# Kernel tuning notes

Hardware: AMD Instinct MI355X
Metric: run time of the kernel (lower is better)

Reference implementation:

```python
import jax, jax.numpy as jnp
import numpy as np
from jax import lax

B, S, D, H = 4, 1024, 1024, 16
DK = D // H


def setup_inputs() -> dict:
    key = jax.random.key(0)
    ks = jax.random.split(key, 8)
    s = 0.02
    return {
        "text_embeddings": jax.random.normal(ks[0], (B, S, D), jnp.float32),
        "text_mask": jnp.ones((B, S), jnp.int32),
        "W_G": jax.random.normal(ks[1], (D, D), jnp.float32) * s,
        "b_G": jnp.zeros((D,), jnp.float32),
        "Wq": jax.random.normal(ks[2], (D, D), jnp.float32) * s,
        "bq": jnp.zeros((D,), jnp.float32),
        "Wk": jax.random.normal(ks[3], (D, D), jnp.float32) * s,
        "bk": jnp.zeros((D,), jnp.float32),
        "conv_w": jax.random.normal(ks[4], (D, H, 3), jnp.float32) * s,
        "conv_b": jnp.zeros((D,), jnp.float32),
    }


def _rope_tables(seq_len, dk):
    # interleaved sinusoidal tables, each value repeated twice along feature dim
    pos = jnp.arange(seq_len, dtype=jnp.float32)[:, None]            # [S,1]
    inv = jnp.power(10000.0, -2.0 * jnp.arange(dk // 2, dtype=jnp.float32) / dk)
    ang = pos * inv                                                   # [S,DK/2]
    cos_pos = jnp.repeat(jnp.cos(ang), 2, axis=-1)[None, None]        # [1,1,S,DK]
    sin_pos = jnp.repeat(jnp.sin(ang), 2, axis=-1)[None, None]
    return cos_pos, sin_pos


def reference(text_embeddings, text_mask, W_G, b_G, Wq, bq, Wk, bk, conv_w, conv_b):
    b, s, d = text_embeddings.shape
    g = text_embeddings @ W_G + b_G                                   # [B,S,D]
    q = (g @ Wq + bq).reshape(b, s, H, DK).transpose(0, 2, 1, 3)      # [B,H,S,DK]
    k = (g @ Wk + bk).reshape(b, s, H, DK).transpose(0, 2, 1, 3)

    cos_pos, sin_pos = _rope_tables(s, DK)
    # NOTE: query rotation uses +q_odd (module does NOT negate for q), key uses -k_odd
    qw2 = jnp.stack([q[..., 1::2], q[..., ::2]], axis=-1).reshape(q.shape)
    qw = q * cos_pos + qw2 * sin_pos
    kw2 = jnp.stack([-k[..., 1::2], k[..., ::2]], axis=-1).reshape(k.shape)
    kw = k * cos_pos + kw2 * sin_pos

    scores = jnp.einsum("bhqd,bhkd->bhqk", qw, kw) / np.float32(np.sqrt(DK))
    mask = text_mask[:, None, None, :]                                # [B,1,1,S]
    scores = jnp.where(mask == 0, jnp.float32(-1e9), scores)
    p_attn = jax.nn.softmax(scores, axis=-1)                          # [B,H,S,S]

    row0 = p_attn[:, :, 0, :]                                         # [B,H,S]
    conv = lax.conv_general_dilated(
        row0, conv_w, window_strides=(1,), padding=[(1, 1)],
        dimension_numbers=("NCH", "OIH", "NCH"))                      # [B,D,S]
    return jax.nn.relu(conv + conv_b[None, :, None])
```

## Files before the change

### kernel.cpp

```cpp
#include <hip/hip_runtime.h>
#include <math.h>

#define B_  4
#define S_  1024
#define D_  1024
#define H_  16
#define DK_ 64
#define M_  (B_ * S_)

typedef __bf16 bf16x8 __attribute__((ext_vector_type(8)));
typedef float  f32x4  __attribute__((ext_vector_type(4)));

__device__ __forceinline__ unsigned short f2bf(float f) {
  unsigned u = __builtin_bit_cast(unsigned, f);
  u = (u + 0x7FFFu + ((u >> 16) & 1u)) >> 16;
  return (unsigned short)u;
}
__device__ __forceinline__ float bf2f(unsigned short h) {
  unsigned u = ((unsigned)h) << 16;
  return __builtin_bit_cast(float, u);
}

__device__ __forceinline__ void gl_lds16(const void* g, void* lds) {
  __builtin_amdgcn_global_load_lds(
      (const __attribute__((address_space(1))) unsigned int*)(unsigned long long)g,
      (__attribute__((address_space(3))) unsigned int*)(unsigned int)(unsigned long long)lds,
      16, 0, 0);
}

__global__ __launch_bounds__(256) void prep_kernel(
    const float* __restrict__ X, const float* __restrict__ W_G,
    const float* __restrict__ Wk, const float* __restrict__ bG,
    unsigned short* __restrict__ WGbf, unsigned short* __restrict__ WkT,
    float* __restrict__ partG, float* __restrict__ partB) {
  __shared__ float tle[32][33];
  __shared__ float gs2[4][32];
  __shared__ float bgs[32];
  const int blk = blockIdx.x;
  const int tid = threadIdx.x;

  if (blk < 512) {
    const int i = (blk * 256 + tid) * 2;
    const float4 v0 = ((const float4*)W_G)[i];
    const float4 v1 = ((const float4*)W_G)[i + 1];
    ushort4 h0, h1;
    h0.x = f2bf(v0.x); h0.y = f2bf(v0.y); h0.z = f2bf(v0.z); h0.w = f2bf(v0.w);
    h1.x = f2bf(v1.x); h1.y = f2bf(v1.y); h1.z = f2bf(v1.z); h1.w = f2bf(v1.w);
    ((ushort4*)WGbf)[i] = h0;
    ((ushort4*)WGbf)[i + 1] = h1;
  } else if (blk < 1536) {
    const int t = blk - 512;
    const int k0 = (t & 31) * 32;
    const int n0 = (t >> 5) * 32;
    const int tx = tid & 31;
    const int ty = tid >> 5;
#pragma unroll
    for (int r = 0; r < 32; r += 8)
      tle[ty + r][tx] = Wk[(size_t)(k0 + ty + r) * 1024 + n0 + tx];
    __syncthreads();
#pragma unroll
    for (int r = 0; r < 32; r += 8)
      WkT[(size_t)(n0 + ty + r) * 1024 + k0 + tx] = f2bf(tle[tx][ty + r]);
  } else if (blk < 1664) {
    const int bl = blk - 1536;
    const int sg = bl >> 2;
    const int mg = bl & 3;
    if (tid < 128) {
      const int b = tid >> 5, kk = tid & 31;
      gs2[b][kk] = X[(size_t)b * S_ * D_ + sg * 32 + kk];
    }
    __syncthreads();
    const int mid = mg * 256 + tid;
    float a0 = 0.f, a1 = 0.f, a2 = 0.f, a3 = 0.f;
#pragma unroll
    for (int kk = 0; kk < 32; ++kk) {
      const float w = W_G[(size_t)(sg * 32 + kk) * 1024 + mid];
      a0 = fmaf(gs2[0][kk], w, a0);
      a1 = fmaf(gs2[1][kk], w, a1);
      a2 = fmaf(gs2[2][kk], w, a2);
      a3 = fmaf(gs2[3][kk], w, a3);
    }
    partG[(size_t)(sg * 4 + 0) * 1024 + mid] = a0;
    partG[(size_t)(sg * 4 + 1) * 1024 + mid] = a1;
    partG[(size_t)(sg * 4 + 2) * 1024 + mid] = a2;
    partG[(size_t)(sg * 4 + 3) * 1024 + mid] = a3;
  } else {
    const int bl = blk - 1664;
    const int sl = bl >> 2;
    const int ng = bl & 3;
    if (tid < 32) bgs[tid] = bG[sl * 32 + tid];
    __syncthreads();
    const int n = ng * 256 + tid;
    float a = 0.f;
#pragma unroll
    for (int kk = 0; kk < 32; ++kk)
      a = fmaf(bgs[kk], Wk[(size_t)(sl * 32 + kk) * 1024 + n], a);
    partB[(size_t)sl * 1024 + n] = a;
  }
}

#define GM 64
#define GN 128

__global__ __launch_bounds__(256) void gemm_bf16(
    const unsigned short* __restrict__ A, const unsigned short* __restrict__ BT,
    const float* __restrict__ bias, unsigned short* __restrict__ C,
    const int mShift, const int nGemmBlocks,
    const float* __restrict__ Wq, float* __restrict__ part,
    const float* __restrict__ partG, const float* __restrict__ bG,
    const float* __restrict__ partB, const float* __restrict__ bk,
    float* __restrict__ biasK,
    const float* __restrict__ X, unsigned short* __restrict__ Xbf,
    float* __restrict__ tab,
    const float* __restrict__ bq, const int* __restrict__ mask,
    float* __restrict__ scores, float* __restrict__ mS) {
  __shared__ __align__(16) unsigned short As[2][GM * 32];
  __shared__ __align__(16) unsigned short Bs[2][GN * 32];
  __shared__ float gs[4][32];
  __shared__ float q0s[128];
  __shared__ float sc[64][9];

  const int flat = blockIdx.x;
  const int tid  = threadIdx.x;

  if (flat >= nGemmBlocks) {
    const int eb = flat - nGemmBlocks;
    if (eb < 128) {
      const int slab = eb >> 2;
      const int n = (eb & 3) * 256 + tid;
      if (tid < 128) {
        const int b = tid >> 5, kk = tid & 31;
        float v = bG[slab * 32 + kk];
        const float* pg = partG + (size_t)b * 1024 + slab * 32 + kk;
#pragma unroll
        for (int sg = 0; sg < 32; ++sg) v += pg[(size_t)sg * 4096];
        gs[b][kk] = v;
      }
      __syncthreads();
      float a0 = 0.f, a1 = 0.f, a2 = 0.f, a3 = 0.f;
#pragma unroll
      for (int kk = 0; kk < 32; ++kk) {
        const float w = Wq[(size_t)(slab * 32 + kk) * D_ + n];
        a0 = fmaf(gs[0][kk], w, a0);
        a1 = fmaf(gs[1][kk], w, a1);
        a2 = fmaf(gs[2][kk], w, a2);
        a3 = fmaf(gs[3][kk], w, a3);
      }
      part[(size_t)(slab * 4 + 0) * D_ + n] = a0;
      part[(size_t)(slab * 4 + 1) * D_ + n] = a1;
      part[(size_t)(slab * 4 + 2) * D_ + n] = a2;
      part[(size_t)(slab * 4 + 3) * D_ + n] = a3;
    } else if (eb < 132) {
      const int n = (eb - 128) * 256 + tid;
      float v = bk[n];
#pragma unroll
      for (int sl = 0; sl < 32; ++sl) v += partB[(size_t)sl * 1024 + n];
      biasK[n] = v;
    } else if (eb < 260) {
      const int idx = (eb - 132) * 256 + tid;
      const int s = idx >> 5, j = idx & 31;
      const float inv = (float)exp(-(double)j * (9.210340371976182736 / 32.0));
      float sn, c;
      sincosf((float)s * inv, &sn, &c);
      tab[(size_t)s * 64 + 2 * j] = c;
      tab[(size_t)s * 64 + 2 * j + 1] = sn;
    } else {
      const int i = ((eb - 260) * 256 + tid) * 2;
      const float4 v0 = ((const float4*)X)[i];
      const float4 v1 = ((const float4*)X)[i + 1];
      ushort4 h0, h1;
      h0.x = f2bf(v0.x); h0.y = f2bf(v0.y); h0.z = f2bf(v0.z); h0.w = f2bf(v0.w);
      h1.x = f2bf(v1.x); h1.y = f2bf(v1.y); h1.z = f2bf(v1.z); h1.w = f2bf(v1.w);
      ((ushort4*)Xbf)[i] = h0;
      ((ushort4*)Xbf)[i + 1] = h1;
    }
    return;
  }

  const int bx = flat >> mShift;
  const int by = flat & ((1 << mShift) - 1);
  const int wv   = tid >> 6;
  const int lane = tid & 63;
  const int m0 = by * GM;
  const int n0 = bx * GN;

  if (scores && tid < 128) {
    const int nq = n0 + tid;
    float v = bq[nq];
#pragma unroll
    for (int sl2 = 0; sl2 < 32; ++sl2)
      v += part[(size_t)(sl2 * 4 + (m0 >> 10)) * D_ + nq];
    q0s[tid] = v;
  }

  const int colOff = (lane & 3) * 8;
  const size_t aOff  = (size_t)(m0 + 16 * wv + (lane >> 2)) * 1024 + colOff;
  const size_t bOff0 = (size_t)(n0 + 32 * wv + (lane >> 2)) * 1024 + colOff;
  const size_t bOff1 = bOff0 + (size_t)16 * 1024;

  const int l15  = lane & 15;
  const int quad = lane >> 4;

  f32x4 acc[4][2];
#pragma unroll
  for (int i = 0; i < 4; ++i)
#pragma unroll
    for (int j = 0; j < 2; ++j) acc[i][j] = (f32x4){0.f, 0.f, 0.f, 0.f};

#pragma unroll 1
  for (int k0 = 0; k0 < 1024; k0 += 64) {
    __syncthreads();
#pragma unroll
    for (int ks = 0; ks < 2; ++ks) {
      gl_lds16(A  + aOff  + k0 + ks * 32, &As[ks][wv * 512]);
      gl_lds16(BT + bOff0 + k0 + ks * 32, &Bs[ks][wv * 1024]);
      gl_lds16(BT + bOff1 + k0 + ks * 32, &Bs[ks][wv * 1024 + 512]);
    }
    __syncthreads();

#pragma unroll
    for (int ks = 0; ks < 2; ++ks) {
      bf16x8 af[4], bfr[2];
#pragma unroll
      for (int mi = 0; mi < 4; ++mi)
        af[mi] = *(const bf16x8*)(&As[ks][(mi * 16 + l15) * 32 + quad * 8]);
#pragma unroll
      for (int ni = 0; ni < 2; ++ni)
        bfr[ni] =
            *(const bf16x8*)(&Bs[ks][(wv * 32 + ni * 16 + l15) * 32 + quad * 8]);
#pragma unroll
      for (int mi = 0; mi < 4; ++mi)
#pragma unroll
        for (int ni = 0; ni < 2; ++ni)
          acc[mi][ni] = __builtin_amdgcn_mfma_f32_16x16x32_bf16(
              af[mi], bfr[ni], acc[mi][ni], 0, 0, 0);
    }
  }

  if (scores) {
    const int b_i   = m0 >> 10;
    const int sbase = m0 & 1023;
#pragma unroll
    for (int ni = 0; ni < 2; ++ni) {
      const int n_loc = wv * 32 + ni * 16 + l15;
      const float bv  = bias[n0 + n_loc];
      const float q0a = q0s[n_loc];
      const float q0b = q0s[n_loc ^ 1];
      const float sq  = (n_loc & 1) ? -q0b : q0b;
      const int j2    = (n_loc & 63) & ~1;
#pragma unroll
      for (int mi = 0; mi < 4; ++mi) {
#pragma unroll
        for (int r = 0; r < 4; ++r) {
          const int s_loc = mi * 16 + quad * 4 + r;
          const float2 cs =
              *(const float2*)(tab + (size_t)(sbase + s_loc) * 64 + j2);
          const float coef = q0a * cs.x + sq * cs.y;
          float v = (acc[mi][ni][r] + bv) * coef;
          v += __shfl_xor(v, 1);
          v += __shfl_xor(v, 2);
          v += __shfl_xor(v, 4);
          v += __shfl_xor(v, 8);
          if (l15 == 0) sc[s_loc][wv * 2 + ni] = v;
        }
      }
    }
    __syncthreads();
    if (tid < 128) {
      const int h_loc = tid >> 6;
      const int s_loc = tid & 63;
      const float* row = sc[s_loc];
      float dot = (row[h_loc * 4 + 0] + row[h_loc * 4 + 1]) +
                  (row[h_loc * 4 + 2] + row[h_loc * 4 + 3]);
      dot *= 0.125f;
      const int s = sbase + s_loc;
      if (mask[b_i * S_ + s] == 0) dot = -1e9f;
      const int bh = b_i * H_ + (bx * 2 + h_loc);
      scores[(size_t)bh * S_ + s] = dot;
      float mx = dot;
#pragma unroll
      for (int off = 16; off >= 1; off >>= 1)
        mx = fmaxf(mx, __shfl_xor(mx, off, 32));
      float e = expf(dot - mx);
#pragma unroll
      for (int off = 16; off >= 1; off >>= 1) e += __shfl_xor(e, off, 32);
      if ((s_loc & 31) == 0) {
        const int ch = ((by & 15) << 1) + (s_loc >> 5);
        mS[((size_t)bh * 32 + ch) * 2 + 0] = mx;
        mS[((size_t)bh * 32 + ch) * 2 + 1] = e;
      }
    }
    return;
  }

#pragma unroll
  for (int ni = 0; ni < 2; ++ni) {
    const int n = n0 + wv * 32 + ni * 16 + l15;
    const float bv = bias ? bias[n] : 0.f;
#pragma unroll
    for (int mi = 0; mi < 4; ++mi) {
#pragma unroll
      for (int r = 0; r < 4; ++r) {
        const int m = m0 + mi * 16 + quad * 4 + r;
        C[(size_t)m * 1024 + n] = f2bf(acc[mi][ni][r] + bv);
      }
    }
  }
}

__global__ __launch_bounds__(256) void conv_norm_relu_kernel(
    const float* __restrict__ scores, const float* __restrict__ mS,
    const float* __restrict__ cw, const float* __restrict__ cb,
    float* __restrict__ out) {
  const int b  = blockIdx.y;
  const int s0 = blockIdx.x * 128;
  const int o0 = blockIdx.z * 64;
  const int tid = threadIdx.x;
  const int tx = tid & 15;
  const int ty = tid >> 4;

  __shared__ float msh[16], ish[16];
  __shared__ __align__(16) float wT[48][68];
  __shared__ float cbs[64];
  __shared__ __align__(16) float pm[16][196];

  if (tid < 16) {
    const int bh = b * H_ + tid;
    float m = -3e38f;
#pragma unroll
    for (int c = 0; c < 32; ++c)
      m = fmaxf(m, mS[(size_t)(bh * 32 + c) * 2]);
    float S = 0.f;
#pragma unroll
    for (int c = 0; c < 32; ++c)
      S += mS[(size_t)(bh * 32 + c) * 2 + 1] *
           expf(mS[(size_t)(bh * 32 + c) * 2] - m);
    msh[tid] = m;
    ish[tid] = 1.f / S;
  }
  for (int i = tid; i < 64 * 48; i += 256) {
    const int ol = i / 48, ct = i % 48;
    wT[ct][ol] = cw[(size_t)(o0 + ol) * 48 + ct];
  }
  if (tid < 64) cbs[tid] = cb[o0 + tid];
  __syncthreads();

  for (int i = tid; i < 16 * 130; i += 256) {
    const int c = i / 130, col = i % 130;
    const int gs = s0 - 1 + col;
    pm[c][12 * (col >> 3) + (col & 7)] =
        (gs >= 0 && gs < S_)
            ? expf(scores[(size_t)(b * H_ + c) * S_ + gs] - msh[c]) * ish[c]
            : 0.f;
  }
  __syncthreads();

  float acc[4][8];
#pragma unroll
  for (int i = 0; i < 4; ++i) {
    const float cv = cbs[ty * 4 + i];
#pragma unroll
    for (int j = 0; j < 8; ++j) acc[i][j] = cv;
  }

#pragma unroll
  for (int c = 0; c < 16; ++c) {
    float pl[10];
    const float* base = &pm[c][12 * tx];
    *(float4*)(pl + 0) = *(const float4*)(base + 0);
    *(float4*)(pl + 4) = *(const float4*)(base + 4);
    *(float2*)(pl + 8) = *(const float2*)(&pm[c][12 * (tx + 1)]);
#pragma unroll
    for (int t = 0; t < 3; ++t) {
      float w[4];
      *(float4*)w = *(const float4*)&wT[c * 3 + t][ty * 4];
#pragma unroll
      for (int i = 0; i < 4; ++i)
#pragma unroll
        for (int j = 0; j < 8; ++j)
          acc[i][j] = fmaf(pl[j + t], w[i], acc[i][j]);
    }
  }

#pragma unroll
  for (int i = 0; i < 4; ++i) {
    float* orow =
        out + ((size_t)b * D_ + o0 + ty * 4 + i) * S_ + s0 + tx * 8;
    float4 v0, v1;
    v0.x = fmaxf(acc[i][0], 0.f); v0.y = fmaxf(acc[i][1], 0.f);
    v0.z = fmaxf(acc[i][2], 0.f); v0.w = fmaxf(acc[i][3], 0.f);
    v1.x = fmaxf(acc[i][4], 0.f); v1.y = fmaxf(acc[i][5], 0.f);
    v1.z = fmaxf(acc[i][6], 0.f); v1.w = fmaxf(acc[i][7], 0.f);
    *(float4*)(orow + 0) = v0;
    *(float4*)(orow + 4) = v1;
  }
}

extern "C" void kernel_launch(void* const* d_in, const int* in_sizes, int n_in,
                              void* d_out, int out_size, void* d_ws,
                              size_t ws_size, hipStream_t stream) {
  const float* x    = (const float*)d_in[0];
  const int*   mask = (const int*)d_in[1];
  const float* W_G  = (const float*)d_in[2];
  const float* b_G  = (const float*)d_in[3];
  const float* Wq   = (const float*)d_in[4];
  const float* bq   = (const float*)d_in[5];
  const float* Wk   = (const float*)d_in[6];
  const float* bk   = (const float*)d_in[7];
  const float* cw   = (const float*)d_in[8];
  const float* cb   = (const float*)d_in[9];
  float* out = (float*)d_out;

  char* ws = (char*)d_ws;
  unsigned short* Xbf  = (unsigned short*)(ws);
  unsigned short* WkT  = (unsigned short*)(ws + (16u << 20));
  unsigned short* WGbf = (unsigned short*)(ws + (18u << 20));
  unsigned short* WfT  = (unsigned short*)(ws + (20u << 20));
  float* part   = (float*)(ws + (22u << 20));
  float* partG  = (float*)(ws + (22u << 20) + (512u << 10));
  float* partB  = (float*)(ws + (23u << 20));
  float* biasK  = (float*)(ws + (23u << 20) + (128u << 10));
  float* ropeT  = (float*)(ws + (23u << 20) + (256u << 10));
  float* scores = (float*)(ws + (23u << 20) + (512u << 10));
  float* mS     = (float*)(ws + (23u << 20) + (768u << 10));

  prep_kernel<<<1792, 256, 0, stream>>>(x, W_G, Wk, b_G, WGbf, WkT,
                                        partG, partB);
  gemm_bf16<<<2436, 256, 0, stream>>>(WkT, WGbf, nullptr, WfT, 4, 128,
                                      Wq, part, partG, b_G, partB, bk, biasK,
                                      x, Xbf, ropeT,
                                      nullptr, nullptr, nullptr, nullptr);
  gemm_bf16<<<512, 256, 0, stream>>>(Xbf, WfT, biasK, nullptr, 6, 512,
                                     nullptr, part, nullptr, nullptr,
                                     nullptr, nullptr, nullptr,
                                     nullptr, nullptr, ropeT,
                                     bq, mask, scores, mS);
  conv_norm_relu_kernel<<<dim3(8, B_, 16), 256, 0, stream>>>(
      scores, mS, cw, cb, out);
}
```

Baseline: 150.7 us.

## Double-buffer LDS tiles in bf16 GEMM to overlap global loads with MFMA

Doubles the shared-memory A/B tile buffers and prefetches the next k-tile via global_load_lds while computing on the current one, using explicit vmcnt waits and raw s_barrier in place of __syncthreads. The goal is to hide global-memory latency behind MFMA work in the main GEMM loop. It doubles LDS usage, which may lower occupancy, and depends on the manual vmcnt(6) count matching the six loads issued per stage.

New measurement: 140.3 us. 1.07x faster.

```diff
diff --git a/kernel.cpp b/kernel.cpp
--- a/kernel.cpp
+++ b/kernel.cpp
@@ -114,8 +114,8 @@
     float* __restrict__ tab,
     const float* __restrict__ bq, const int* __restrict__ mask,
     float* __restrict__ scores, float* __restrict__ mS) {
-  __shared__ __align__(16) unsigned short As[2][GM * 32];
-  __shared__ __align__(16) unsigned short Bs[2][GN * 32];
+  __shared__ __align__(16) unsigned short As[2][2][GM * 32];
+  __shared__ __align__(16) unsigned short Bs[2][2][GN * 32];
   __shared__ float gs[4][32];
   __shared__ float q0s[128];
   __shared__ float sc[64][9];
@@ -207,27 +207,39 @@
 #pragma unroll
     for (int j = 0; j < 2; ++j) acc[i][j] = (f32x4){0.f, 0.f, 0.f, 0.f};
 
+  auto STAGE = [&](int bufi, int kk) {
+#pragma unroll
+    for (int ks = 0; ks < 2; ++ks) {
+      gl_lds16(A  + aOff  + kk + ks * 32, &As[bufi][ks][wv * 512]);
+      gl_lds16(BT + bOff0 + kk + ks * 32, &Bs[bufi][ks][wv * 1024]);
+      gl_lds16(BT + bOff1 + kk + ks * 32, &Bs[bufi][ks][wv * 1024 + 512]);
+    }
+  };
+
+  STAGE(0, 0);
+
 #pragma unroll 1
-  for (int k0 = 0; k0 < 1024; k0 += 64) {
-    __syncthreads();
-#pragma unroll
-    for (int ks = 0; ks < 2; ++ks) {
-      gl_lds16(A  + aOff  + k0 + ks * 32, &As[ks][wv * 512]);
-      gl_lds16(BT + bOff0 + k0 + ks * 32, &Bs[ks][wv * 1024]);
-      gl_lds16(BT + bOff1 + k0 + ks * 32, &Bs[ks][wv * 1024 + 512]);
-    }
-    __syncthreads();
+  for (int t = 0; t < 16; ++t) {
+    const int cur = t & 1;
+    if (t < 15) {
+      STAGE(cur ^ 1, (t + 1) * 64);
+      asm volatile("s_waitcnt vmcnt(6)" ::: "memory");
+    } else {
+      asm volatile("s_waitcnt vmcnt(0)" ::: "memory");
+    }
+    __builtin_amdgcn_s_barrier();
+    __builtin_amdgcn_sched_barrier(0);
 
 #pragma unroll
     for (int ks = 0; ks < 2; ++ks) {
       bf16x8 af[4], bfr[2];
 #pragma unroll
       for (int mi = 0; mi < 4; ++mi)
-        af[mi] = *(const bf16x8*)(&As[ks][(mi * 16 + l15) * 32 + quad * 8]);
+        af[mi] = *(const bf16x8*)(&As[cur][ks][(mi * 16 + l15) * 32 + quad * 8]);
 #pragma unroll
       for (int ni = 0; ni < 2; ++ni)
-        bfr[ni] =
-            *(const bf16x8*)(&Bs[ks][(wv * 32 + ni * 16 + l15) * 32 + quad * 8]);
+        bfr[ni] = *(const bf16x8*)(
+            &Bs[cur][ks][(wv * 32 + ni * 16 + l15) * 32 + quad * 8]);
 #pragma unroll
       for (int mi = 0; mi < 4; ++mi)
 #pragma unroll
@@ -235,6 +247,8 @@
           acc[mi][ni] = __builtin_amdgcn_mfma_f32_16x16x32_bf16(
               af[mi], bfr[ni], acc[mi][ni], 0, 0, 0);
     }
+    __builtin_amdgcn_sched_barrier(0);
+    __builtin_amdgcn_s_barrier();
   }
 
   if (scores) {
```
